# Kernel optimization log

Measured on AMD Instinct MI355X. Metric: run time of the kernel, lower is better.

## Reference

```python
import jax, jax.numpy as jnp
import numpy as np

N = 100000   # nodes
E = 1600000  # edges (avg degree 16)
D = 64       # feature dim (in_dim)


def setup_inputs() -> dict:
    key = jax.random.key(0)
    k1, k2, k3, k4, k5 = jax.random.split(key, 5)
    h = jax.random.normal(k1, (N, D), dtype=jnp.float32)
    dnorm = jax.random.uniform(k2, (N,), dtype=jnp.float32)  # deg^-1/2 proxy
    # xavier_normal_(gain=1.414) for Linear(2D, 1): std = gain*sqrt(2/(fan_in+fan_out))
    std = 1.414 * np.sqrt(2.0 / (2 * D + 1))
    gate_w = jax.random.normal(k3, (1, 2 * D), dtype=jnp.float32) * std
    gate_b = jnp.zeros((1,), dtype=jnp.float32)
    src = jax.random.randint(k4, (E,), 0, N, dtype=jnp.int32)
    dst = jax.random.randint(k5, (E,), 0, N, dtype=jnp.int32)
    return {"h": h, "dnorm": dnorm, "gate_w": gate_w, "gate_b": gate_b,
            "src": src, "dst": dst}


def reference(h, dnorm, gate_w, gate_b, src, dst):
    # gate(cat[h_dst, h_src]) == h_dst @ W[:, :D].T + h_src @ W[:, D:].T + b
    w_dst = gate_w[0, :D]  # [D]
    w_src = gate_w[0, D:]  # [D]
    h_src = h[src]                                        # [E, D] gather
    g = jnp.tanh(h[dst] @ w_dst + h_src @ w_src + gate_b[0])  # [E]
    e = g * dnorm[dst] * dnorm[src]                       # [E] (dropout p=0 -> identity)
    # u_mul_e + sum: z[v] = sum_{(u->v)} h[u] * e
    z = jax.ops.segment_sum(h_src * e[:, None], dst, num_segments=N)  # [N, D]
    return z
```

## Files before the change

kernel.cpp:

```cpp
#include <hip/hip_runtime.h>
#include <hip/hip_bf16.h>

#define D 64
#define BKT_SHIFT 7
#define BKT_NODES 128
#define NB_CNT 1024
#define DSPLIT_T 1024
#define DSPLIT_E 4096
#define CAP 2560

__device__ __forceinline__ unsigned short f2bf(float x) {
    unsigned u = __float_as_uint(x);
    unsigned r = 0x7fffu + ((u >> 16) & 1u);
    return (unsigned short)((u + r) >> 16);
}

template<bool MAKE_BF16>
__global__ void fal_precompute(const float* __restrict__ h,
                               const float* __restrict__ dnorm,
                               const float* __restrict__ gate_w,
                               const float* __restrict__ gate_b,
                               float2* __restrict__ sd,
                               float2* __restrict__ ss,
                               unsigned short* __restrict__ hb,
                               int N) {
    int tid  = threadIdx.x;
    int lane = tid & 63;
    int wave = tid >> 6;
    int grp  = lane >> 4;
    int gl   = lane & 15;

    int node = blockIdx.x * 16 + wave * 4 + grp;
    int nc   = node < N ? node : N - 1;

    const float4* h4 = (const float4*)h;
    const float4* w4 = (const float4*)gate_w;

    float4 hv  = h4[nc * 16 + gl];
    float4 wd  = w4[gl];
    float4 wsr = w4[16 + gl];

    if (MAKE_BF16 && node < N) {
        ushort4 p = make_ushort4(f2bf(hv.x), f2bf(hv.y), f2bf(hv.z), f2bf(hv.w));
        *(ushort4*)&hb[(size_t)node * D + gl * 4] = p;
    }

    float a = hv.x * wd.x + hv.y * wd.y + hv.z * wd.z + hv.w * wd.w;
    float b = hv.x * wsr.x + hv.y * wsr.y + hv.z * wsr.z + hv.w * wsr.w;

    for (int off = 1; off < 16; off <<= 1) {
        a += __shfl_xor(a, off, 64);
        b += __shfl_xor(b, off, 64);
    }

    if (gl == 0 && node < N) {
        float dn = dnorm[node];
        sd[node] = make_float2(a + gate_b[0], dn);
        ss[node] = make_float2(b, dn);
    }
}

__global__ __launch_bounds__(DSPLIT_T) void fal_multisplit(
        const int* __restrict__ src,
        const int* __restrict__ dst,
        int* __restrict__ bcursor,
        unsigned* __restrict__ pk_bin,
        int E, int nb) {
    __shared__ int lcount[NB_CNT];
    __shared__ int lscan[NB_CNT];
    __shared__ int gofs[NB_CNT];
    __shared__ int wsum16[16];
    __shared__ unsigned s_pk[DSPLIT_E];
    __shared__ int s_gpos[DSPLIT_E];

    int tid  = threadIdx.x;
    int lane = tid & 63;
    int w    = tid >> 6;
    lcount[tid] = 0;
    __syncthreads();

    int E4 = E >> 2;
    int i4 = blockIdx.x * DSPLIT_T + tid;

    int srcs[4], dsts[4], lr[4];
    bool act = (i4 < E4);
    if (act) {
        int4 s4 = ((const int4*)src)[i4];
        int4 d4 = ((const int4*)dst)[i4];
        srcs[0] = s4.x; srcs[1] = s4.y; srcs[2] = s4.z; srcs[3] = s4.w;
        dsts[0] = d4.x; dsts[1] = d4.y; dsts[2] = d4.z; dsts[3] = d4.w;
        #pragma unroll
        for (int j = 0; j < 4; ++j)
            lr[j] = atomicAdd(&lcount[dsts[j] >> BKT_SHIFT], 1);
    }
    __syncthreads();

    int v = lcount[tid];
    for (int off = 1; off < 64; off <<= 1) {
        int t = __shfl_up(v, off, 64);
        if (lane >= off) v += t;
    }
    if (lane == 63) wsum16[w] = v;
    __syncthreads();
    if (tid < 16) {
        int s = wsum16[tid];
        for (int off = 1; off < 16; off <<= 1) {
            int t = __shfl_up(s, off, 64);
            if (tid >= off) s += t;
        }
        wsum16[tid] = s;
    }
    __syncthreads();
    lscan[tid] = v + (w ? wsum16[w - 1] : 0);

    if (tid < nb) {
        int c = lcount[tid];
        int rel = c ? atomicAdd(&bcursor[tid], c) : 0;
        gofs[tid] = tid * CAP + rel;
    }
    __syncthreads();

    if (act) {
        #pragma unroll
        for (int j = 0; j < 4; ++j) {
            int b = dsts[j] >> BKT_SHIFT;
            int lpos = (lscan[b] - lcount[b]) + lr[j];
            unsigned dl = (unsigned)(dsts[j] & (BKT_NODES - 1));
            s_pk[lpos] = (dl << 20) | (unsigned)srcs[j];
            int gp = gofs[b] + lr[j];
            s_gpos[lpos] = (gp < (b + 1) * CAP) ? gp : -1;
        }
    }
    __syncthreads();

    int total = lscan[NB_CNT - 1];
    for (int t = tid; t < total; t += DSPLIT_T) {
        int g = s_gpos[t];
        if (g >= 0) pk_bin[g] = s_pk[t];
    }
}

template<bool BF16>
__global__ __launch_bounds__(512) void fal_bucket_process(
        const float* __restrict__ h,
        const unsigned short* __restrict__ hb,
        const float2* __restrict__ sd,
        const float2* __restrict__ ss,
        const int* __restrict__ bcursor,
        const unsigned* __restrict__ pk_bin,
        float* __restrict__ z, int N) {
    __shared__ unsigned s_pk[CAP];
    __shared__ unsigned s_srt[CAP];
    __shared__ float    s_esc[CAP];
    __shared__ float2   sdl[BKT_NODES];
    __shared__ int nhist[BKT_NODES];
    __shared__ int nbase[BKT_NODES];
    __shared__ int ncur[BKT_NODES];
    __shared__ int wsum8[8];

    int b    = blockIdx.x;
    int tid  = threadIdx.x;
    int lane = tid & 63;
    int w    = tid >> 6;

    if (tid < BKT_NODES) {
        nhist[tid] = 0;
        int node = b * BKT_NODES + tid;
        sdl[tid] = (node < N) ? sd[node] : make_float2(0.f, 0.f);
    }
    __syncthreads();

    int cnt = min(bcursor[b], CAP);
    const unsigned* bin = pk_bin + (size_t)b * CAP;

    for (int t = tid; t < cnt; t += 512) {
        unsigned pk = bin[t];
        s_pk[t] = pk;
        atomicAdd(&nhist[pk >> 20], 1);
    }
    __syncthreads();

    int myh = (tid < BKT_NODES) ? nhist[tid] : 0;
    int v = myh;
    for (int off = 1; off < 64; off <<= 1) {
        int t = __shfl_up(v, off, 64);
        if (lane >= off) v += t;
    }
    if (lane == 63) wsum8[w] = v;
    __syncthreads();
    if (tid < 8) {
        int s2 = wsum8[tid];
        for (int off = 1; off < 8; off <<= 1) {
            int t = __shfl_up(s2, off, 64);
            if (tid >= off) s2 += t;
        }
        wsum8[tid] = s2;
    }
    __syncthreads();
    if (tid < BKT_NODES) {
        int incl = v + (w ? wsum8[w - 1] : 0);
        nbase[tid] = incl - myh;
        ncur[tid]  = 0;
    }
    __syncthreads();

    for (int t = tid; t < cnt; t += 512) {
        unsigned pk = s_pk[t];
        int dl = (int)(pk >> 20);
        int sn = (int)(pk & 0xFFFFFu);
        int r  = atomicAdd(&ncur[dl], 1);
        float2 sv = ss[sn];
        float2 dv = sdl[dl];
        float esc = tanhf(dv.x + sv.x) * dv.y * sv.y;
        int p = nbase[dl] + r;
        s_srt[p] = pk;
        s_esc[p] = esc;
    }
    __syncthreads();

    int oct  = tid >> 3;
    int sdim = tid & 7;

    #pragma unroll
    for (int ni = 0; ni < BKT_NODES / 64; ++ni) {
        int dl   = oct + ni * 64;
        int seg0 = nbase[dl];
        int dg   = nhist[dl];

        float acc[8];
        #pragma unroll
        for (int i = 0; i < 8; ++i) acc[i] = 0.0f;

        int k = 0;
        for (; k + 2 <= dg; k += 2) {
            unsigned p0 = s_srt[seg0 + k];
            unsigned p1 = s_srt[seg0 + k + 1];
            float    e0 = s_esc[seg0 + k];
            float    e1 = s_esc[seg0 + k + 1];
            int s0 = (int)(p0 & 0xFFFFFu);
            int s1 = (int)(p1 & 0xFFFFFu);
            if (BF16) {
                uint4 a0 = *(const uint4*)&hb[(size_t)s0 * D + sdim * 8];
                uint4 a1 = *(const uint4*)&hb[(size_t)s1 * D + sdim * 8];
                acc[0] = fmaf(__uint_as_float(a0.x << 16),         e0, acc[0]);
                acc[1] = fmaf(__uint_as_float(a0.x & 0xffff0000u), e0, acc[1]);
                acc[2] = fmaf(__uint_as_float(a0.y << 16),         e0, acc[2]);
                acc[3] = fmaf(__uint_as_float(a0.y & 0xffff0000u), e0, acc[3]);
                acc[4] = fmaf(__uint_as_float(a0.z << 16),         e0, acc[4]);
                acc[5] = fmaf(__uint_as_float(a0.z & 0xffff0000u), e0, acc[5]);
                acc[6] = fmaf(__uint_as_float(a0.w << 16),         e0, acc[6]);
                acc[7] = fmaf(__uint_as_float(a0.w & 0xffff0000u), e0, acc[7]);
                acc[0] = fmaf(__uint_as_float(a1.x << 16),         e1, acc[0]);
                acc[1] = fmaf(__uint_as_float(a1.x & 0xffff0000u), e1, acc[1]);
                acc[2] = fmaf(__uint_as_float(a1.y << 16),         e1, acc[2]);
                acc[3] = fmaf(__uint_as_float(a1.y & 0xffff0000u), e1, acc[3]);
                acc[4] = fmaf(__uint_as_float(a1.z << 16),         e1, acc[4]);
                acc[5] = fmaf(__uint_as_float(a1.z & 0xffff0000u), e1, acc[5]);
                acc[6] = fmaf(__uint_as_float(a1.w << 16),         e1, acc[6]);
                acc[7] = fmaf(__uint_as_float(a1.w & 0xffff0000u), e1, acc[7]);
            } else {
                const float4* hp0 = (const float4*)&h[(size_t)s0 * D + sdim * 8];
                const float4* hp1 = (const float4*)&h[(size_t)s1 * D + sdim * 8];
                float4 q0 = hp0[0], q1 = hp0[1], q2 = hp1[0], q3 = hp1[1];
                acc[0] = fmaf(q0.x, e0, acc[0]); acc[1] = fmaf(q0.y, e0, acc[1]);
                acc[2] = fmaf(q0.z, e0, acc[2]); acc[3] = fmaf(q0.w, e0, acc[3]);
                acc[4] = fmaf(q1.x, e0, acc[4]); acc[5] = fmaf(q1.y, e0, acc[5]);
                acc[6] = fmaf(q1.z, e0, acc[6]); acc[7] = fmaf(q1.w, e0, acc[7]);
                acc[0] = fmaf(q2.x, e1, acc[0]); acc[1] = fmaf(q2.y, e1, acc[1]);
                acc[2] = fmaf(q2.z, e1, acc[2]); acc[3] = fmaf(q2.w, e1, acc[3]);
                acc[4] = fmaf(q3.x, e1, acc[4]); acc[5] = fmaf(q3.y, e1, acc[5]);
                acc[6] = fmaf(q3.z, e1, acc[6]); acc[7] = fmaf(q3.w, e1, acc[7]);
            }
        }
        if (k < dg) {
            unsigned p0 = s_srt[seg0 + k];
            float    e0 = s_esc[seg0 + k];
            int s0 = (int)(p0 & 0xFFFFFu);
            if (BF16) {
                uint4 a0 = *(const uint4*)&hb[(size_t)s0 * D + sdim * 8];
                acc[0] = fmaf(__uint_as_float(a0.x << 16),         e0, acc[0]);
                acc[1] = fmaf(__uint_as_float(a0.x & 0xffff0000u), e0, acc[1]);
                acc[2] = fmaf(__uint_as_float(a0.y << 16),         e0, acc[2]);
                acc[3] = fmaf(__uint_as_float(a0.y & 0xffff0000u), e0, acc[3]);
                acc[4] = fmaf(__uint_as_float(a0.z << 16),         e0, acc[4]);
                acc[5] = fmaf(__uint_as_float(a0.z & 0xffff0000u), e0, acc[5]);
                acc[6] = fmaf(__uint_as_float(a0.w << 16),         e0, acc[6]);
                acc[7] = fmaf(__uint_as_float(a0.w & 0xffff0000u), e0, acc[7]);
            } else {
                const float4* hp0 = (const float4*)&h[(size_t)s0 * D + sdim * 8];
                float4 q0 = hp0[0], q1 = hp0[1];
                acc[0] = fmaf(q0.x, e0, acc[0]); acc[1] = fmaf(q0.y, e0, acc[1]);
                acc[2] = fmaf(q0.z, e0, acc[2]); acc[3] = fmaf(q0.w, e0, acc[3]);
                acc[4] = fmaf(q1.x, e0, acc[4]); acc[5] = fmaf(q1.y, e0, acc[5]);
                acc[6] = fmaf(q1.z, e0, acc[6]); acc[7] = fmaf(q1.w, e0, acc[7]);
            }
        }

        int node = b * BKT_NODES + dl;
        if (node < N) {
            float4* zp = (float4*)&z[(size_t)node * D + sdim * 8];
            zp[0] = make_float4(acc[0], acc[1], acc[2], acc[3]);
            zp[1] = make_float4(acc[4], acc[5], acc[6], acc[7]);
        }
    }
}

extern "C" void kernel_launch(void* const* d_in, const int* in_sizes, int n_in,
                              void* d_out, int out_size, void* d_ws, size_t ws_size,
                              hipStream_t stream) {
    const float* h      = (const float*)d_in[0];
    const float* dnorm  = (const float*)d_in[1];
    const float* gate_w = (const float*)d_in[2];
    const float* gate_b = (const float*)d_in[3];
    const int*   src    = (const int*)d_in[4];
    const int*   dst    = (const int*)d_in[5];
    float*       z      = (float*)d_out;

    int N  = in_sizes[1];
    int E  = in_sizes[4];
    int nb = (N + BKT_NODES - 1) >> BKT_SHIFT;

    char* ws0 = (char*)d_ws;
    size_t off = 0;
    auto alloc = [&](size_t bytes) {
        char* p = ws0 + off;
        off += (bytes + 15) & ~(size_t)15;
        return p;
    };
    float2*   sd      = (float2*)alloc((size_t)N * sizeof(float2));
    float2*   ss      = (float2*)alloc((size_t)N * sizeof(float2));
    int*      bcursor = (int*)alloc((size_t)nb * sizeof(int));
    unsigned* pk_bin  = (unsigned*)alloc((size_t)nb * CAP * sizeof(unsigned));
    unsigned short* hb = (unsigned short*)(ws0 + off);
    size_t need_with_hb = off + (size_t)N * D * sizeof(unsigned short);
    bool use_bf16 = (ws_size >= need_with_hb);

    hipMemsetAsync(bcursor, 0, (size_t)nb * sizeof(int), stream);

    if (use_bf16)
        fal_precompute<true><<<(N + 15) / 16, 256, 0, stream>>>(
            h, dnorm, gate_w, gate_b, sd, ss, hb, N);
    else
        fal_precompute<false><<<(N + 15) / 16, 256, 0, stream>>>(
            h, dnorm, gate_w, gate_b, sd, ss, hb, N);

    fal_multisplit<<<(E + DSPLIT_E - 1) / DSPLIT_E, DSPLIT_T, 0, stream>>>(
        src, dst, bcursor, pk_bin, E, nb);

    if (use_bf16)
        fal_bucket_process<true><<<nb, 512, 0, stream>>>(
            h, hb, sd, ss, bcursor, pk_bin, z, N);
    else
        fal_bucket_process<false><<<nb, 512, 0, stream>>>(
            h, hb, sd, ss, bcursor, pk_bin, z, N);
}
```

Before: 168.5 us.

## Balance bucket gather by splitting edge ranges evenly across 8-thread groups

The gather phase of the bucket kernel now gives each 8-thread group an equal contiguous slice of the sorted edge list instead of one destination node each, which removes the imbalance from skewed in-degrees. Segments that cross slice boundaries are combined with atomic adds after those rows are zeroed, and interior segments are written directly. Edge index and scale are packed into one swizzled uint2 in shared memory, and the next source row is prefetched one step ahead. This adds atomics and branchy boundary logic and makes the float summation order nondeterministic.

```diff
diff --git a/kernel.cpp b/kernel.cpp
--- a/kernel.cpp
+++ b/kernel.cpp
@@ -150,8 +150,7 @@
         const unsigned* __restrict__ pk_bin,
         float* __restrict__ z, int N) {
     __shared__ unsigned s_pk[CAP];
-    __shared__ unsigned s_srt[CAP];
-    __shared__ float    s_esc[CAP];
+    __shared__ uint2    s_srt[CAP];
     __shared__ float2   sdl[BKT_NODES];
     __shared__ int nhist[BKT_NODES];
     __shared__ int nbase[BKT_NODES];
@@ -203,6 +202,9 @@
         ncur[tid]  = 0;
     }
     __syncthreads();
+
+    int L = (cnt + 63) >> 6;
+    L = (L + 1) & ~1;
 
     for (int t = tid; t < cnt; t += 512) {
         unsigned pk = s_pk[t];
@@ -213,95 +215,119 @@
         float2 dv = sdl[dl];
         float esc = tanhf(dv.x + sv.x) * dv.y * sv.y;
         int p = nbase[dl] + r;
-        s_srt[p] = pk;
-        s_esc[p] = esc;
-    }
-    __syncthreads();
+        s_srt[p ^ ((p >> 4) & 15)] = make_uint2(pk, __float_as_uint(esc));
+    }
 
     int oct  = tid >> 3;
     int sdim = tid & 7;
+    int cbase = sdim * 8;
 
     #pragma unroll
-    for (int ni = 0; ni < BKT_NODES / 64; ++ni) {
-        int dl   = oct + ni * 64;
-        int seg0 = nbase[dl];
-        int dg   = nhist[dl];
+    for (int ni = 0; ni < 2; ++ni) {
+        int dl = oct + ni * 64;
+        int node = b * BKT_NODES + dl;
+        if (node < N) {
+            int dg = nhist[dl];
+            bool needz;
+            if (dg == 0) {
+                needz = true;
+            } else {
+                int s = nbase[dl];
+                needz = (s / L) != ((s + dg - 1) / L);
+            }
+            if (needz) {
+                float4 z4 = make_float4(0.f, 0.f, 0.f, 0.f);
+                float4* zp = (float4*)&z[(size_t)node * D + cbase];
+                zp[0] = z4; zp[1] = z4;
+            }
+        }
+    }
+    __syncthreads();
+
+    int t0 = oct * L;
+    int t1 = min(t0 + L, cnt);
+    if (t0 < t1) {
+        auto closeSeg = [&](unsigned dl_, const float* a, bool direct) {
+            int node = b * BKT_NODES + (int)dl_;
+            float* zr = &z[(size_t)node * D + cbase];
+            if (direct) {
+                ((float4*)zr)[0] = make_float4(a[0], a[1], a[2], a[3]);
+                ((float4*)zr)[1] = make_float4(a[4], a[5], a[6], a[7]);
+            } else {
+                #pragma unroll
+                for (int i = 0; i < 8; ++i) unsafeAtomicAdd(&zr[i], a[i]);
+            }
+        };
+
+        int sw0 = t0 ^ ((t0 >> 4) & 15);
+        uint2 eC = s_srt[sw0];
+        unsigned cur = eC.x >> 20;
+        bool started_in = true;
+        if (t0 > 0) {
+            int swp = (t0 - 1) ^ (((t0 - 1) >> 4) & 15);
+            started_in = ((s_srt[swp].x >> 20) != cur);
+        }
+
+        uint4 rowC;
+        float4 q0C, q1C;
+        {
+            size_t base = (size_t)(eC.x & 0xFFFFFu) * D + cbase;
+            if constexpr (BF16) rowC = *(const uint4*)&hb[base];
+            else { const float4* hp = (const float4*)&h[base]; q0C = hp[0]; q1C = hp[1]; }
+        }
 
         float acc[8];
         #pragma unroll
-        for (int i = 0; i < 8; ++i) acc[i] = 0.0f;
-
-        int k = 0;
-        for (; k + 2 <= dg; k += 2) {
-            unsigned p0 = s_srt[seg0 + k];
-            unsigned p1 = s_srt[seg0 + k + 1];
-            float    e0 = s_esc[seg0 + k];
-            float    e1 = s_esc[seg0 + k + 1];
-            int s0 = (int)(p0 & 0xFFFFFu);
-            int s1 = (int)(p1 & 0xFFFFFu);
-            if (BF16) {
-                uint4 a0 = *(const uint4*)&hb[(size_t)s0 * D + sdim * 8];
-                uint4 a1 = *(const uint4*)&hb[(size_t)s1 * D + sdim * 8];
-                acc[0] = fmaf(__uint_as_float(a0.x << 16),         e0, acc[0]);
-                acc[1] = fmaf(__uint_as_float(a0.x & 0xffff0000u), e0, acc[1]);
-                acc[2] = fmaf(__uint_as_float(a0.y << 16),         e0, acc[2]);
-                acc[3] = fmaf(__uint_as_float(a0.y & 0xffff0000u), e0, acc[3]);
-                acc[4] = fmaf(__uint_as_float(a0.z << 16),         e0, acc[4]);
-                acc[5] = fmaf(__uint_as_float(a0.z & 0xffff0000u), e0, acc[5]);
-                acc[6] = fmaf(__uint_as_float(a0.w << 16),         e0, acc[6]);
-                acc[7] = fmaf(__uint_as_float(a0.w & 0xffff0000u), e0, acc[7]);
-                acc[0] = fmaf(__uint_as_float(a1.x << 16),         e1, acc[0]);
-                acc[1] = fmaf(__uint_as_float(a1.x & 0xffff0000u), e1, acc[1]);
-                acc[2] = fmaf(__uint_as_float(a1.y << 16),         e1, acc[2]);
-                acc[3] = fmaf(__uint_as_float(a1.y & 0xffff0000u), e1, acc[3]);
-                acc[4] = fmaf(__uint_as_float(a1.z << 16),         e1, acc[4]);
-                acc[5] = fmaf(__uint_as_float(a1.z & 0xffff0000u), e1, acc[5]);
-                acc[6] = fmaf(__uint_as_float(a1.w << 16),         e1, acc[6]);
-                acc[7] = fmaf(__uint_as_float(a1.w & 0xffff0000u), e1, acc[7]);
+        for (int i = 0; i < 8; ++i) acc[i] = 0.f;
+
+        #pragma unroll 2
+        for (int t = t0; t < t1; ++t) {
+            uint2 e = eC;
+            uint4 row; float4 q0, q1;
+            if constexpr (BF16) row = rowC; else { q0 = q0C; q1 = q1C; }
+
+            int tn = t + 1;
+            if (tn < t1) {
+                int swn = tn ^ ((tn >> 4) & 15);
+                eC = s_srt[swn];
+                size_t base = (size_t)(eC.x & 0xFFFFFu) * D + cbase;
+                if constexpr (BF16) rowC = *(const uint4*)&hb[base];
+                else { const float4* hp = (const float4*)&h[base]; q0C = hp[0]; q1C = hp[1]; }
+            }
+
+            unsigned dl = e.x >> 20;
+            if (dl != cur) {
+                closeSeg(cur, acc, started_in);
+                started_in = true;
+                cur = dl;
+                #pragma unroll
+                for (int i = 0; i < 8; ++i) acc[i] = 0.f;
+            }
+
+            float esc = __uint_as_float(e.y);
+            if constexpr (BF16) {
+                acc[0] = fmaf(__uint_as_float(row.x << 16),         esc, acc[0]);
+                acc[1] = fmaf(__uint_as_float(row.x & 0xffff0000u), esc, acc[1]);
+                acc[2] = fmaf(__uint_as_float(row.y << 16),         esc, acc[2]);
+                acc[3] = fmaf(__uint_as_float(row.y & 0xffff0000u), esc, acc[3]);
+                acc[4] = fmaf(__uint_as_float(row.z << 16),         esc, acc[4]);
+                acc[5] = fmaf(__uint_as_float(row.z & 0xffff0000u), esc, acc[5]);
+                acc[6] = fmaf(__uint_as_float(row.w << 16),         esc, acc[6]);
+                acc[7] = fmaf(__uint_as_float(row.w & 0xffff0000u), esc, acc[7]);
             } else {
-                const float4* hp0 = (const float4*)&h[(size_t)s0 * D + sdim * 8];
-                const float4* hp1 = (const float4*)&h[(size_t)s1 * D + sdim * 8];
-                float4 q0 = hp0[0], q1 = hp0[1], q2 = hp1[0], q3 = hp1[1];
-                acc[0] = fmaf(q0.x, e0, acc[0]); acc[1] = fmaf(q0.y, e0, acc[1]);
-                acc[2] = fmaf(q0.z, e0, acc[2]); acc[3] = fmaf(q0.w, e0, acc[3]);
-                acc[4] = fmaf(q1.x, e0, acc[4]); acc[5] = fmaf(q1.y, e0, acc[5]);
-                acc[6] = fmaf(q1.z, e0, acc[6]); acc[7] = fmaf(q1.w, e0, acc[7]);
-                acc[0] = fmaf(q2.x, e1, acc[0]); acc[1] = fmaf(q2.y, e1, acc[1]);
-                acc[2] = fmaf(q2.z, e1, acc[2]); acc[3] = fmaf(q2.w, e1, acc[3]);
-                acc[4] = fmaf(q3.x, e1, acc[4]); acc[5] = fmaf(q3.y, e1, acc[5]);
-                acc[6] = fmaf(q3.z, e1, acc[6]); acc[7] = fmaf(q3.w, e1, acc[7]);
-            }
-        }
-        if (k < dg) {
-            unsigned p0 = s_srt[seg0 + k];
-            float    e0 = s_esc[seg0 + k];
-            int s0 = (int)(p0 & 0xFFFFFu);
-            if (BF16) {
-                uint4 a0 = *(const uint4*)&hb[(size_t)s0 * D + sdim * 8];
-                acc[0] = fmaf(__uint_as_float(a0.x << 16),         e0, acc[0]);
-                acc[1] = fmaf(__uint_as_float(a0.x & 0xffff0000u), e0, acc[1]);
-                acc[2] = fmaf(__uint_as_float(a0.y << 16),         e0, acc[2]);
-                acc[3] = fmaf(__uint_as_float(a0.y & 0xffff0000u), e0, acc[3]);
-                acc[4] = fmaf(__uint_as_float(a0.z << 16),         e0, acc[4]);
-                acc[5] = fmaf(__uint_as_float(a0.z & 0xffff0000u), e0, acc[5]);
-                acc[6] = fmaf(__uint_as_float(a0.w << 16),         e0, acc[6]);
-                acc[7] = fmaf(__uint_as_float(a0.w & 0xffff0000u), e0, acc[7]);
-            } else {
-                const float4* hp0 = (const float4*)&h[(size_t)s0 * D + sdim * 8];
-                float4 q0 = hp0[0], q1 = hp0[1];
-                acc[0] = fmaf(q0.x, e0, acc[0]); acc[1] = fmaf(q0.y, e0, acc[1]);
-                acc[2] = fmaf(q0.z, e0, acc[2]); acc[3] = fmaf(q0.w, e0, acc[3]);
-                acc[4] = fmaf(q1.x, e0, acc[4]); acc[5] = fmaf(q1.y, e0, acc[5]);
-                acc[6] = fmaf(q1.z, e0, acc[6]); acc[7] = fmaf(q1.w, e0, acc[7]);
-            }
-        }
-
-        int node = b * BKT_NODES + dl;
-        if (node < N) {
-            float4* zp = (float4*)&z[(size_t)node * D + sdim * 8];
-            zp[0] = make_float4(acc[0], acc[1], acc[2], acc[3]);
-            zp[1] = make_float4(acc[4], acc[5], acc[6], acc[7]);
-        }
+                acc[0] = fmaf(q0.x, esc, acc[0]); acc[1] = fmaf(q0.y, esc, acc[1]);
+                acc[2] = fmaf(q0.z, esc, acc[2]); acc[3] = fmaf(q0.w, esc, acc[3]);
+                acc[4] = fmaf(q1.x, esc, acc[4]); acc[5] = fmaf(q1.y, esc, acc[5]);
+                acc[6] = fmaf(q1.z, esc, acc[6]); acc[7] = fmaf(q1.w, esc, acc[7]);
+            }
+        }
+
+        bool ended = true;
+        if (t1 < cnt) {
+            int swn = t1 ^ ((t1 >> 4) & 15);
+            ended = ((s_srt[swn].x >> 20) != cur);
+        }
+        closeSeg(cur, acc, started_in && ended);
     }
 }
 
```

Result: slower. 314.5 us (+86.6%).
